# Kernel optimization log

Hardware: AMD Instinct MI355X
Metric: run time of the kernel (lower is better)

## Reference

```python
import jax, jax.numpy as jnp
import numpy as np

B, S, H, NH, HD = 1, 2048, 768, 12, 64   # batch, seq, hidden, heads, head_dim
W = 256                                   # one-sided window (attention_window=512)
NC = S // W                               # query chunks of width W
L, FF, V, G = 12, 3072, 50265, 1          # layers, ffn, vocab, num global tokens (CLS)
HID, EMB = 768, 256                       # head dense size, output embedding size
SCALE = 1.0 / np.sqrt(HD).astype(np.float32)
EPS = 1e-5

def _ln(x, s, b):
    mu = x.mean(-1, keepdims=True)
    xm = x - mu
    v = (xm * xm).mean(-1, keepdims=True)
    return xm * jax.lax.rsqrt(v + EPS) * s + b

def _forward(input_ids, attention_mask, global_attention_mask,
             word_emb, pos_emb, emb_ln_s, emb_ln_b,
             Wq, bq, Wk, bk, Wv, bv, Wqg, bqg, Wkg, bkg, Wvg, bvg, Wo, bo,
             ln1_s, ln1_b, Wf1, bf1, Wf2, bf2, ln2_s, ln2_b,
             dense_w, dense_b, out_w, out_b):
    h = word_emb[input_ids] + pos_emb[None]            # [B,S,H]
    h = _ln(h, emb_ln_s, emb_ln_b)

    key_ok = attention_mask.astype(bool)               # [B,S]
    is_glb = global_attention_mask.astype(bool)        # [B,S]

    # chunked sliding-window machinery: queries in NC chunks of W, each sees 3W keys
    j = jnp.arange(3 * W); qi = jnp.arange(W); c = jnp.arange(NC)
    rel = j[None, :] - qi[:, None]
    band_ok = (rel >= 0) & (rel <= 2 * W)              # |key-query| <= W  -> [W,3W]
    kpos = c[:, None, None] * W + j[None, None, :] - W # abs key position [NC,1,3W]
    in_range = (kpos >= 0) & (kpos < S)
    kposc = jnp.clip(kpos, 0, S - 1)
    # HF removes global tokens from the windowed band (they get dedicated columns)
    kmask = key_ok[:, kposc] & ~is_glb[:, kposc]       # [B,NC,1,3W]
    band_mask = band_ok[None, None] & in_range[None] & kmask          # [B,NC,W,3W]
    gcol_mask = jnp.broadcast_to(key_ok[:, None, None, :G], (B, NC, W, G))
    full_mask = jnp.concatenate([gcol_mask, band_mask], -1)[:, None]  # [B,1,NC,W,G+3W]
    kidx = c[:, None] * W + j[None, :]                 # gather into padded keys [NC,3W]

    def step(h, p):
        q = ((h @ p['Wq'] + p['bq']).reshape(B, NC, W, NH, HD)) * SCALE
        k = (h @ p['Wk'] + p['bk']).reshape(B, S, NH, HD)
        v = (h @ p['Wv'] + p['bv']).reshape(B, S, NH, HD)
        k_ch = jnp.pad(k, ((0, 0), (W, W), (0, 0), (0, 0)))[:, kidx]  # [B,NC,3W,NH,HD]
        v_ch = jnp.pad(v, ((0, 0), (W, W), (0, 0), (0, 0)))[:, kidx]
        s_band = jnp.einsum('bcqnd,bcknd->bncqk', q, k_ch)            # [B,NH,NC,W,3W]
        s_glob = jnp.einsum('bcqnd,bgnd->bncqg', q, k[:, :G])         # [B,NH,NC,W,G]
        scores = jnp.concatenate([s_glob, s_band], -1)
        probs = jax.nn.softmax(jnp.where(full_mask, scores, -1e9), -1)
        pg, pb = probs[..., :G], probs[..., G:]
        out = (jnp.einsum('bncqk,bcknd->bcqnd', pb, v_ch)
               + jnp.einsum('bncqg,bgnd->bcqnd', pg, v[:, :G]))
        out = out.reshape(B, S, NH, HD)
        # global tokens: full attention with dedicated global projections (HF semantics)
        hg = h[:, :G]
        qg = ((hg @ p['Wqg'] + p['bqg']).reshape(B, G, NH, HD)) * SCALE
        kg = (h @ p['Wkg'] + p['bkg']).reshape(B, S, NH, HD)
        vg = (h @ p['Wvg'] + p['bvg']).reshape(B, S, NH, HD)
        sg = jnp.einsum('bgnd,bsnd->bngs', qg, kg)
        ag = jax.nn.softmax(jnp.where(key_ok[:, None, None, :], sg, -1e9), -1)
        og = jnp.einsum('bngs,bsnd->bgnd', ag, vg)
        out = out.at[:, :G].set(og)
        attn = out.reshape(B, S, H) @ p['Wo'] + p['bo']
        h2 = _ln(h + attn, p['ln1_s'], p['ln1_b'])
        ff = jax.nn.gelu(h2 @ p['Wf1'] + p['bf1'], approximate=False) @ p['Wf2'] + p['bf2']
        return _ln(h2 + ff, p['ln2_s'], p['ln2_b']), None

    params = dict(Wq=Wq, bq=bq, Wk=Wk, bk=bk, Wv=Wv, bv=bv, Wqg=Wqg, bqg=bqg,
                  Wkg=Wkg, bkg=bkg, Wvg=Wvg, bvg=bvg, Wo=Wo, bo=bo,
                  ln1_s=ln1_s, ln1_b=ln1_b, Wf1=Wf1, bf1=bf1, Wf2=Wf2, bf2=bf2,
                  ln2_s=ln2_s, ln2_b=ln2_b)
    h, _ = jax.lax.scan(step, h, params)
    pooled = h[:, 0]                                   # CLS token
    y = jnp.tanh(pooled @ dense_w + dense_b)           # dropout = identity (eval)
    return y @ out_w + out_b                           # [B,EMB]

def setup_inputs() -> dict:
    key = jax.random.key(0)
    it = iter(jax.random.split(key, 16))
    def nrm(shape, sd=0.02):
        return jax.random.normal(next(it), shape, jnp.float32) * sd
    return dict(
        input_ids=jax.random.randint(next(it), (B, S), 0, V),
        attention_mask=jnp.ones((B, S), jnp.int32),
        global_attention_mask=jnp.zeros((B, S), jnp.int32).at[:, 0].set(1),
        word_emb=nrm((V, H)), pos_emb=nrm((S, H)),
        emb_ln_s=jnp.ones((H,)), emb_ln_b=jnp.zeros((H,)),
        Wq=nrm((L, H, H)), bq=jnp.zeros((L, H)),
        Wk=nrm((L, H, H)), bk=jnp.zeros((L, H)),
        Wv=nrm((L, H, H)), bv=jnp.zeros((L, H)),
        Wqg=nrm((L, H, H)), bqg=jnp.zeros((L, H)),
        Wkg=nrm((L, H, H)), bkg=jnp.zeros((L, H)),
        Wvg=nrm((L, H, H)), bvg=jnp.zeros((L, H)),
        Wo=nrm((L, H, H)), bo=jnp.zeros((L, H)),
        ln1_s=jnp.ones((L, H)), ln1_b=jnp.zeros((L, H)),
        Wf1=nrm((L, H, FF)), bf1=jnp.zeros((L, FF)),
        Wf2=nrm((L, FF, H)), bf2=jnp.zeros((L, H)),
        ln2_s=jnp.ones((L, H)), ln2_b=jnp.zeros((L, H)),
        dense_w=nrm((H, HID)), dense_b=jnp.zeros((HID,)),
        out_w=nrm((HID, EMB)), out_b=jnp.zeros((EMB,)),
    )

def reference(input_ids, attention_mask, global_attention_mask,
              word_emb, pos_emb, emb_ln_s, emb_ln_b,
              Wq, bq, Wk, bk, Wv, bv, Wqg, bqg, Wkg, bkg, Wvg, bvg, Wo, bo,
              ln1_s, ln1_b, Wf1, bf1, Wf2, bf2, ln2_s, ln2_b,
              dense_w, dense_b, out_w, out_b):
    return _forward(input_ids, attention_mask, global_attention_mask,
                    word_emb, pos_emb, emb_ln_s, emb_ln_b,
                    Wq, bq, Wk, bk, Wv, bv, Wqg, bqg, Wkg, bkg, Wvg, bvg, Wo, bo,
                    ln1_s, ln1_b, Wf1, bf1, Wf2, bf2, ln2_s, ln2_b,
                    dense_w, dense_b, out_w, out_b)
```

## Files before the change

### kernel.cpp

```cpp
#include <hip/hip_runtime.h>
#include <hip/hip_bf16.h>

typedef __hip_bfloat16 bf16;
using bf16x8 = __attribute__((ext_vector_type(8))) short;
using f32x4  = __attribute__((ext_vector_type(4))) float;

#define kNEG 1.0e9f

__device__ __forceinline__ float b2f(bf16 x){ return __bfloat162float(x); }
__device__ __forceinline__ bf16  f2b(float x){ return __float2bfloat16(x); }

#define GLDS16(gp, lp) __builtin_amdgcn_global_load_lds( \
    (const __attribute__((address_space(1))) void*)(gp), \
    (__attribute__((address_space(3))) void*)(lp), 16, 0, 0)

__device__ __forceinline__ void unpack8(uint4 u, float* f){
  f[0]=__uint_as_float(u.x<<16); f[1]=__uint_as_float(u.x&0xffff0000u);
  f[2]=__uint_as_float(u.y<<16); f[3]=__uint_as_float(u.y&0xffff0000u);
  f[4]=__uint_as_float(u.z<<16); f[5]=__uint_as_float(u.z&0xffff0000u);
  f[6]=__uint_as_float(u.w<<16); f[7]=__uint_as_float(u.w&0xffff0000u);
}

__global__ __launch_bounds__(256)
void embed_ln(const int* __restrict__ ids, const float* __restrict__ wemb,
              const float* __restrict__ pemb, const float* __restrict__ lns,
              const float* __restrict__ lnb, float* __restrict__ hout,
              bf16* __restrict__ hbout)
{
  const int row = blockIdx.x;
  const int tid = threadIdx.x;
  const int wave = tid >> 6, lane = tid & 63;
  const int id = ids[row];
  float x[3];
  #pragma unroll
  for (int p=0;p<3;p++){
    int i = tid + p*256;
    x[p] = wemb[(size_t)id*768 + i] + pemb[(size_t)row*768 + i];
  }
  float s1 = x[0]+x[1]+x[2];
  float s2 = x[0]*x[0]+x[1]*x[1]+x[2]*x[2];
  #pragma unroll
  for (int m=32;m>=1;m>>=1){ s1 += __shfl_xor(s1,m); s2 += __shfl_xor(s2,m); }
  __shared__ float red[8];
  if (lane==0){ red[wave]=s1; red[4+wave]=s2; }
  __syncthreads();
  s1 = red[0]+red[1]+red[2]+red[3];
  s2 = red[4]+red[5]+red[6]+red[7];
  float mu = s1*(1.0f/768.0f);
  float var = s2*(1.0f/768.0f) - mu*mu;
  float rs = rsqrtf(var + 1e-5f);
  #pragma unroll
  for (int p=0;p<3;p++){
    int i = tid + p*256;
    float y = (x[p]-mu)*rs*lns[i] + lnb[i];
    hout[(size_t)row*768+i] = y;
    hbout[(size_t)row*768+i] = f2b(y);
  }
}

__global__ __launch_bounds__(256)
void add_ln(const float* __restrict__ res, const float* __restrict__ d0,
            const float* __restrict__ d1,
            const float* __restrict__ lns, const float* __restrict__ lnb,
            float* __restrict__ hout, bf16* __restrict__ hbout)
{
  const int row = blockIdx.x;
  const int tid = threadIdx.x;
  const int wave = tid >> 6, lane = tid & 63;
  float x[3];
  #pragma unroll
  for (int p=0;p<3;p++){
    int i = tid + p*256;
    size_t idx = (size_t)row*768+i;
    x[p] = res[idx] + d0[idx] + d1[idx];
  }
  float s1 = x[0]+x[1]+x[2];
  float s2 = x[0]*x[0]+x[1]*x[1]+x[2]*x[2];
  #pragma unroll
  for (int m=32;m>=1;m>>=1){ s1 += __shfl_xor(s1,m); s2 += __shfl_xor(s2,m); }
  __shared__ float red[8];
  if (lane==0){ red[wave]=s1; red[4+wave]=s2; }
  __syncthreads();
  s1 = red[0]+red[1]+red[2]+red[3];
  s2 = red[4]+red[5]+red[6]+red[7];
  float mu = s1*(1.0f/768.0f);
  float var = s2*(1.0f/768.0f) - mu*mu;
  float rs = rsqrtf(var + 1e-5f);
  #pragma unroll
  for (int p=0;p<3;p++){
    int i = tid + p*256;
    float y = (x[p]-mu)*rs*lns[i] + lnb[i];
    hout[(size_t)row*768+i] = y;
    hbout[(size_t)row*768+i] = f2b(y);
  }
}

__global__ __launch_bounds__(256)
void prep_all(const float* __restrict__ Wq, const float* __restrict__ Wk,
              const float* __restrict__ Wv, const float* __restrict__ Wkg,
              const float* __restrict__ Wvg, const float* __restrict__ Wo,
              const float* __restrict__ Wf1, const float* __restrict__ Wf2,
              const float* __restrict__ bq, const float* __restrict__ bk,
              const float* __restrict__ bv, const float* __restrict__ bkg,
              const float* __restrict__ bvg,
              bf16* __restrict__ WcatT, bf16* __restrict__ WoT,
              bf16* __restrict__ Wf1T, bf16* __restrict__ Wf2T,
              float* __restrict__ bcat)
{
  const int b = blockIdx.x;
  const int l = blockIdx.y;
  const int tid = threadIdx.x;
  const size_t oHH = (size_t)l*768*768;
  const size_t oHF = (size_t)l*768*3072;
  const size_t oH  = (size_t)l*768;
  if (b >= 504) {
    int i = (b-504)*256 + tid;
    int which = i / 768, j = i - which*768;
    float v;
    if      (which==0) v = bq[oH+j] * 0.125f;
    else if (which==1) v = bk[oH+j];
    else if (which==2) v = bv[oH+j];
    else if (which==3) v = bkg[oH+j];
    else               v = bvg[oH+j];
    bcat[(size_t)l*3840 + i] = v;
    return;
  }
  const float* src; bf16* dst; int N, KT64, p0, tk, k0, n0; float scale = 1.0f;
  if (b < 180) {
    int wsel = b/36, tile = b - wsel*36;
    int tkk = tile/3, tn = tile - tkk*3;
    if      (wsel==0){ src=Wq+oHH;  scale=0.125f; }
    else if (wsel==1){ src=Wk+oHH; }
    else if (wsel==2){ src=Wv+oHH; }
    else if (wsel==3){ src=Wkg+oHH; }
    else             { src=Wvg+oHH; }
    dst = WcatT + (size_t)l*5*768*768;
    N=768; KT64=12; k0=tkk*64; n0=tn*256; p0 = wsel*6 + tn*2; tk = tkk;
  } else if (b < 216) {
    int tile = b-180, tkk = tile/3, tn = tile - tkk*3;
    src = Wo+oHH; dst = WoT + (size_t)l*768*768;
    N=768; KT64=12; k0=tkk*64; n0=tn*256; p0 = tn*2; tk = tkk;
  } else if (b < 360) {
    int tile = b-216, tkk = tile/12, tn = tile - tkk*12;
    src = Wf1+oHF; dst = Wf1T + (size_t)l*768*3072;
    N=3072; KT64=12; k0=tkk*64; n0=tn*256; p0 = tn*2; tk = tkk;
  } else {
    int tile = b-360, tkk = tile/3, tn = tile - tkk*3;
    src = Wf2+oHF; dst = Wf2T + (size_t)l*768*3072;
    N=768; KT64=48; k0=tkk*64; n0=tn*256; p0 = tn*2; tk = tkk;
  }

  __shared__ bf16 t[64][264];
  const int wave = tid>>6, lane = tid&63;
  float4 v[16];
  #pragma unroll
  for (int i=0;i<16;i++){
    int r = i*4 + wave;
    v[i] = *(const float4*)&src[(size_t)(k0+r)*N + n0 + lane*4];
  }
  #pragma unroll
  for (int i=0;i<16;i++){
    int r = i*4 + wave;
    union { ushort4 u; bf16 h[4]; } pk;
    pk.h[0]=f2b(v[i].x*scale); pk.h[1]=f2b(v[i].y*scale);
    pk.h[2]=f2b(v[i].z*scale); pk.h[3]=f2b(v[i].w*scale);
    *(ushort4*)&t[r][lane*4] = pk.u;
  }
  __syncthreads();
  const int rr = tid>>1, half = tid&1;
  const int r7 = rr & 7;
  #pragma unroll
  for (int c=0;c<4;c++){
    const int pp = c>>1, tt = c&1;
    union { uint4 u[2]; bf16 h[16]; } pk;
    #pragma unroll
    for (int j=0;j<16;j++)
      pk.h[j] = t[tt*32 + half*16 + j][pp*128 + rr];
    bf16* base = dst + ((size_t)(p0+pp)*KT64 + tk)*8192 + rr*64;
    const int g0 = tt*4 + half*2;
    *(uint4*)(base + (((g0  ) ^ r7)<<3)) = pk.u[0];
    *(uint4*)(base + (((g0+1) ^ r7)<<3)) = pk.u[1];
  }
}

template<int OUTF, int OUTB, int GELU, int KSPLIT, int VT>
__global__ __launch_bounds__(256)
void gemm_bt(const bf16* __restrict__ A, const bf16* __restrict__ Bt,
             const float* __restrict__ bias,
             float* __restrict__ outf, bf16* __restrict__ outb,
             bf16* __restrict__ vt,
             int M, int N, int K)
{
  __shared__ bf16 As[2][128*64];
  __shared__ bf16 Bs[2][128*64];
  const int tid  = threadIdx.x;
  const int lane = tid & 63;
  const int wave = tid >> 6;
  const int wm = wave >> 1, wn = wave & 1;
  const int gx = gridDim.x, nwg = gx*gridDim.y;
  const int w  = blockIdx.y*gx + blockIdx.x;
  const int cpx = nwg >> 3;
  const int sw = (w & 7)*cpx + (w >> 3);
  const int bm = sw % gx, bn = sw / gx;
  const int bz = (KSPLIT>1) ? blockIdx.z : 0;
  const int fr = lane & 15;
  const int fk = lane >> 4;
  const int x7 = fr & 7;
  const int Ks = K / KSPLIT;
  const int nt = Ks >> 6;
  const int kbeg = bz * Ks;
  const int KT64 = K >> 6;

  const bf16* pa[4];
  int ldsA[4];
  #pragma unroll
  for (int i=0;i<4;i++){
    int s = i*256 + tid;
    int row = s >> 3, k8l = s & 7;
    pa[i] = A + (size_t)(bm*128 + row)*K + kbeg + ((k8l ^ (row&7))<<3);
    ldsA[i] = s*8;
  }
  const bf16* pB = Bt + ((size_t)bn*KT64 + (kbeg>>6))*8192;

  f32x4 acc[4][4];
  const f32x4 zero = {0.f,0.f,0.f,0.f};
  #pragma unroll
  for (int i=0;i<4;i++)
    #pragma unroll
    for (int j=0;j<4;j++) acc[i][j] = zero;

  #pragma unroll
  for (int i=0;i<4;i++) GLDS16(pa[i], &As[0][ldsA[i]]);
  #pragma unroll
  for (int i=0;i<4;i++){ int o=(i*256+tid)*8; GLDS16(pB+o, &Bs[0][o]); }
  if (nt > 1) {
    #pragma unroll
    for (int i=0;i<4;i++) GLDS16(pa[i]+64, &As[1][ldsA[i]]);
    #pragma unroll
    for (int i=0;i<4;i++){ int o=(i*256+tid)*8; GLDS16(pB+8192+o, &Bs[1][o]); }
  }

  for (int t = 0; t < nt; ++t) {
    const int cur = t & 1;
    if (t < nt-1) asm volatile("s_waitcnt vmcnt(8)" ::: "memory");
    else          asm volatile("s_waitcnt vmcnt(0)" ::: "memory");
    __builtin_amdgcn_s_barrier();
    __builtin_amdgcn_sched_barrier(0);

    bf16x8 af[2][4], bfr[2][4];
    #pragma unroll
    for (int kk=0;kk<2;kk++){
      #pragma unroll
      for (int m=0;m<4;m++)
        af[kk][m] = *reinterpret_cast<const bf16x8*>(
            &As[cur][(wm*64 + m*16 + fr)*64 + ((((kk<<2)+fk) ^ x7)<<3)]);
      #pragma unroll
      for (int n=0;n<4;n++)
        bfr[kk][n] = *reinterpret_cast<const bf16x8*>(
            &Bs[cur][(wn*64 + n*16 + fr)*64 + ((((kk<<2)+fk) ^ x7)<<3)]);
    }
    #pragma unroll
    for (int kk=0;kk<2;kk++)
      #pragma unroll
      for (int m=0;m<4;m++)
        #pragma unroll
        for (int n=0;n<4;n++)
          acc[m][n] = __builtin_amdgcn_mfma_f32_16x16x32_bf16(af[kk][m], bfr[kk][n], acc[m][n], 0,0,0);

    __builtin_amdgcn_s_barrier();
    __builtin_amdgcn_sched_barrier(0);
    if (t+2 < nt) {
      #pragma unroll
      for (int i=0;i<4;i++) GLDS16(pa[i] + (size_t)(t+2)*64, &As[cur][ldsA[i]]);
      #pragma unroll
      for (int i=0;i<4;i++){ int o=(i*256+tid)*8;
        GLDS16(pB + (size_t)(t+2)*8192 + o, &Bs[cur][o]); }
    }
  }

  const int row0 = bm*128 + wm*64 + (lane>>4)*4;
  const int col0 = bn*128 + wn*64 + fr;
  float* outfz = OUTF ? (outf + (size_t)bz*M*N) : nullptr;
  #pragma unroll
  for (int n=0;n<4;n++){
    const int col = col0 + n*16;
    const float bv = (bz==0) ? bias[col] : 0.f;
    #pragma unroll
    for (int m=0;m<4;m++){
      const int r0 = row0 + m*16;
      union { ushort4 u; bf16 h[4]; } pk;
      #pragma unroll
      for (int r=0;r<4;r++){
        float x = acc[m][n][r] + bv;
        if (GELU) x = 0.5f*x*(1.0f + erff(x*0.70710678118f));
        size_t idx = (size_t)(r0+r)*N + col;
        pk.h[r] = f2b(x);
        if (OUTF) outfz[idx] = x;
        if (OUTB) outb[idx] = pk.h[r];
      }
      if (VT) {
        if (col >= 1536 && col < 2304)
          *(ushort4*)&vt[(size_t)(col-1536)*2048 + r0] = pk.u;
      }
    }
  }
}

__global__ __launch_bounds__(256)
void band_attn(const bf16* __restrict__ qkv, const bf16* __restrict__ Vt,
               const float* __restrict__ h0, const float* __restrict__ Wqg,
               const float* __restrict__ bqg,
               const int* __restrict__ amask, const int* __restrict__ gmask,
               bf16* __restrict__ attn)
{
  const int c = blockIdx.x, n = blockIdx.y, rg = blockIdx.z;
  const int tid = threadIdx.x, wave = tid>>6, lane = tid&63;

  if (rg == 4) {
    if (c != 0) return;
    __shared__ float sg[2048];
    __shared__ float qh[64];
    __shared__ float redg[8];
    __shared__ float partg[4][64];
    {
      const int d = tid & 63;
      const int w = tid >> 6;
      const float* wp = Wqg + (size_t)(w*192)*768 + n*64 + d;
      float a = 0.f;
      #pragma unroll 8
      for (int k=0;k<192;k++) a += h0[w*192+k] * wp[(size_t)k*768];
      partg[w][d] = a;
    }
    __syncthreads();
    if (tid < 64)
      qh[tid] = (partg[0][tid]+partg[1][tid]+partg[2][tid]+partg[3][tid] + bqg[n*64+tid]) * 0.125f;
    __syncthreads();

    float smax = -3.0e38f;
    for (int p=0;p<8;p++){
      int s = p*256 + tid;
      const uint4* kr = (const uint4*)(qkv + (size_t)s*3840 + 2304 + n*64);
      float acc = 0.f;
      #pragma unroll
      for (int d8=0; d8<8; d8++){
        float f[8]; unpack8(kr[d8], f);
        #pragma unroll
        for (int e=0;e<8;e++) acc += f[e]*qh[d8*8+e];
      }
      if (amask[s] == 0) acc = -kNEG;
      sg[s] = acc;
      smax = fmaxf(smax, acc);
    }
    #pragma unroll
    for (int mk=32; mk>=1; mk>>=1) smax = fmaxf(smax, __shfl_xor(smax, mk));
    if (lane==0) redg[wave] = smax;
    __syncthreads();
    smax = fmaxf(fmaxf(redg[0],redg[1]),fmaxf(redg[2],redg[3]));
    float ssum = 0.f;
    for (int p=0;p<8;p++){
      int s = p*256 + tid;
      float e = __expf(sg[s]-smax);
      sg[s] = e;
      ssum += e;
    }
    #pragma unroll
    for (int mk=32; mk>=1; mk>>=1) ssum += __shfl_xor(ssum, mk);
    if (lane==0) redg[4+wave] = ssum;
    __syncthreads();
    float total = redg[4]+redg[5]+redg[6]+redg[7];
    __syncthreads();

    float o0=0.f,o1=0.f,o2=0.f,o3=0.f;
    const int base = wave*512;
    for (int s = base; s < base+512; s+=4){
      o0 += sg[s]   * b2f(qkv[(size_t)s*3840     + 3072 + n*64 + lane]);
      o1 += sg[s+1] * b2f(qkv[(size_t)(s+1)*3840 + 3072 + n*64 + lane]);
      o2 += sg[s+2] * b2f(qkv[(size_t)(s+2)*3840 + 3072 + n*64 + lane]);
      o3 += sg[s+3] * b2f(qkv[(size_t)(s+3)*3840 + 3072 + n*64 + lane]);
    }
    partg[wave][lane] = (o0+o1)+(o2+o3);
    __syncthreads();
    if (tid < 64) {
      float oo = (partg[0][tid]+partg[1][tid]+partg[2][tid]+partg[3][tid]) / total;
      attn[n*64+tid] = f2b(oo);
    }
    return;
  }

  const int fr = lane & 15, fk = lane >> 4;
  const int jj = tid >> 2, seg = tid & 3;

  __shared__ __attribute__((aligned(16))) bf16 q_s[64][72];
  __shared__ __attribute__((aligned(16))) bf16 k_s[2][64][72];
  __shared__ __attribute__((aligned(16))) bf16 vt_s[2][64][72];
  __shared__ __attribute__((aligned(16))) bf16 p_s[4][16][72];
  __shared__ int  okk_s[768];
  __shared__ float kv0[2][64];

  {
    const uint4* src = (const uint4*)(qkv + (size_t)(c*256 + rg*64 + jj)*3840 + n*64 + seg*16);
    *(uint4*)&q_s[jj][seg*16]   = src[0];
    *(uint4*)&q_s[jj][seg*16+8] = src[1];
  }
  #pragma unroll
  for (int p=0;p<3;p++){
    int j = tid + p*256;
    int kpos = c*256 + j - 256;
    int ok = 0;
    if (kpos >= 0 && kpos < 2048) ok = (amask[kpos] != 0) && (gmask[kpos] == 0);
    okk_s[j] = ok;
  }
  if (tid < 64)       kv0[0][tid]    = b2f(qkv[768  + n*64 + tid]);
  else if (tid < 128) kv0[1][tid-64] = b2f(qkv[1536 + n*64 + (tid-64)]);

  auto loadK = [&](int kt, uint4& a, uint4& b){
    int kpos = c*256 + kt*64 + jj - 256;
    int kq = kpos < 0 ? 0 : (kpos > 2047 ? 2047 : kpos);
    const uint4* ks = (const uint4*)(qkv + (size_t)kq*3840 + 768 + n*64 + seg*16);
    a = ks[0]; b = ks[1];
  };
  auto loadV = [&](int kt, uint4& a, uint4& b){
    int base = c*256 + kt*64 - 256;
    int sb = (base < 0 || base > 2048-64) ? 0 : base;
    const uint4* vs = (const uint4*)(Vt + (size_t)(n*64 + jj)*2048 + sb + seg*8);
    a = vs[0]; b = vs[4];
  };

  uint4 ka,kb,va,vb;
  loadK(rg,ka,kb); loadV(rg,va,vb);
  *(uint4*)&k_s[0][jj][seg*16]    = ka;
  *(uint4*)&k_s[0][jj][seg*16+8]  = kb;
  *(uint4*)&vt_s[0][jj][seg*8]    = va;
  *(uint4*)&vt_s[0][jj][seg*8+32] = vb;

  float m[4], l[4];
  f32x4 out[4];
  const f32x4 zero = {0.f,0.f,0.f,0.f};
  #pragma unroll
  for (int r=0;r<4;r++){ m[r] = -kNEG; l[r] = 0.f; }
  #pragma unroll
  for (int dt=0;dt<4;dt++) out[dt] = zero;

  const int kt1 = (rg+8 < 11) ? rg+8 : 11;
  int cur = 0;
  for (int kt = rg; kt <= kt1; kt++) {
    const bool pf = (kt < kt1);
    if (pf){ loadK(kt+1,ka,kb); loadV(kt+1,va,vb); }
    __syncthreads();

    f32x4 s[4];
    #pragma unroll
    for (int ct=0;ct<4;ct++) s[ct] = zero;
    #pragma unroll
    for (int ks=0;ks<2;ks++){
      bf16x8 aq = *reinterpret_cast<const bf16x8*>(&q_s[wave*16 + fr][ks*32 + fk*8]);
      #pragma unroll
      for (int ct=0;ct<4;ct++){
        bf16x8 bk = *reinterpret_cast<const bf16x8*>(&k_s[cur][ct*16 + fr][ks*32 + fk*8]);
        s[ct] = __builtin_amdgcn_mfma_f32_16x16x32_bf16(aq, bk, s[ct], 0,0,0);
      }
    }
    const int qbase = rg*64 + wave*16 + fk*4;
    #pragma unroll
    for (int ct=0;ct<4;ct++){
      int j = kt*64 + ct*16 + fr;
      int okj = okk_s[j];
      #pragma unroll
      for (int r=0;r<4;r++){
        unsigned rel = (unsigned)(j - (qbase + r));
        s[ct][r] = (okj && rel <= 512u) ? s[ct][r] : -kNEG;
      }
    }
    float fac[4], psum[4];
    #pragma unroll
    for (int r=0;r<4;r++){
      float mm = fmaxf(fmaxf(s[0][r], s[1][r]), fmaxf(s[2][r], s[3][r]));
      #pragma unroll
      for (int mk=8; mk>=1; mk>>=1) mm = fmaxf(mm, __shfl_xor(mm, mk));
      float mn = fmaxf(m[r], mm);
      fac[r] = __expf(m[r] - mn);
      m[r] = mn;
      psum[r] = 0.f;
    }
    #pragma unroll
    for (int ct=0;ct<4;ct++){
      #pragma unroll
      for (int r=0;r<4;r++){
        float p = __expf(s[ct][r] - m[r]);
        psum[r] += p;
        p_s[wave][fk*4 + r][ct*16 + fr] = f2b(p);
      }
    }
    #pragma unroll
    for (int r=0;r<4;r++){
      float ts = psum[r];
      #pragma unroll
      for (int mk=8; mk>=1; mk>>=1) ts += __shfl_xor(ts, mk);
      l[r] = l[r]*fac[r] + ts;
    }
    #pragma unroll
    for (int dt=0;dt<4;dt++)
      #pragma unroll
      for (int r=0;r<4;r++) out[dt][r] *= fac[r];
    #pragma unroll
    for (int ks=0;ks<2;ks++){
      bf16x8 ap = *reinterpret_cast<const bf16x8*>(&p_s[wave][fr][ks*32 + fk*8]);
      #pragma unroll
      for (int dt=0;dt<4;dt++){
        bf16x8 bv = *reinterpret_cast<const bf16x8*>(&vt_s[cur][dt*16 + fr][ks*32 + fk*8]);
        out[dt] = __builtin_amdgcn_mfma_f32_16x16x32_bf16(ap, bv, out[dt], 0,0,0);
      }
    }

    if (pf){
      *(uint4*)&k_s[cur^1][jj][seg*16]    = ka;
      *(uint4*)&k_s[cur^1][jj][seg*16+8]  = kb;
      *(uint4*)&vt_s[cur^1][jj][seg*8]    = va;
      *(uint4*)&vt_s[cur^1][jj][seg*8+32] = vb;
      cur ^= 1;
    }
  }

  const bool okg = (amask[0] != 0);
  #pragma unroll
  for (int r=0;r<4;r++){
    const int row16 = fk*4 + r;
    float sp = 0.f;
    #pragma unroll
    for (int e=0;e<4;e++){
      int d = fr*4 + e;
      sp += b2f(q_s[wave*16 + row16][d]) * kv0[0][d];
    }
    #pragma unroll
    for (int mk=8; mk>=1; mk>>=1) sp += __shfl_xor(sp, mk);
    float sg2 = okg ? sp : -kNEG;
    float mn = fmaxf(m[r], sg2);
    float fc = __expf(m[r]-mn);
    float pg = __expf(sg2-mn);
    float lf = l[r]*fc + pg;
    const int srow = c*256 + rg*64 + wave*16 + row16;
    if (srow != 0) {
      #pragma unroll
      for (int dt=0;dt<4;dt++){
        int d = dt*16 + fr;
        float o = (out[dt][r]*fc + pg*kv0[1][d]) / lf;
        attn[(size_t)srow*768 + n*64 + d] = f2b(o);
      }
    }
  }
}

__global__ __launch_bounds__(768)
void head(const float* __restrict__ h0, const float* __restrict__ dw,
          const float* __restrict__ db, const float* __restrict__ ow,
          const float* __restrict__ ob, float* __restrict__ out)
{
  __shared__ float y[768];
  const int tid = threadIdx.x;
  float acc = 0.f;
  #pragma unroll 8
  for (int k=0;k<768;k++) acc += h0[k]*dw[(size_t)k*768 + tid];
  y[tid] = tanhf(acc + db[tid]);
  __syncthreads();
  if (tid < 256) {
    float a = 0.f;
    #pragma unroll 8
    for (int k=0;k<768;k++) a += y[k]*ow[(size_t)k*256 + tid];
    out[tid] = a + ob[tid];
  }
}

extern "C" void kernel_launch(void* const* d_in, const int* in_sizes, int n_in,
                              void* d_out, int out_size, void* d_ws, size_t ws_size,
                              hipStream_t stream)
{
  const int*   ids   = (const int*)d_in[0];
  const int*   amask = (const int*)d_in[1];
  const int*   gmask = (const int*)d_in[2];
  const float* wemb  = (const float*)d_in[3];
  const float* pemb  = (const float*)d_in[4];
  const float* elns  = (const float*)d_in[5];
  const float* elnb  = (const float*)d_in[6];
  const float* Wq    = (const float*)d_in[7];
  const float* bq    = (const float*)d_in[8];
  const float* Wk    = (const float*)d_in[9];
  const float* bk    = (const float*)d_in[10];
  const float* Wv    = (const float*)d_in[11];
  const float* bv    = (const float*)d_in[12];
  const float* Wqg   = (const float*)d_in[13];
  const float* bqg   = (const float*)d_in[14];
  const float* Wkg   = (const float*)d_in[15];
  const float* bkg   = (const float*)d_in[16];
  const float* Wvg   = (const float*)d_in[17];
  const float* bvg   = (const float*)d_in[18];
  const float* Wo    = (const float*)d_in[19];
  const float* bo    = (const float*)d_in[20];
  const float* ln1s  = (const float*)d_in[21];
  const float* ln1b  = (const float*)d_in[22];
  const float* Wf1   = (const float*)d_in[23];
  const float* bf1   = (const float*)d_in[24];
  const float* Wf2   = (const float*)d_in[25];
  const float* bf2   = (const float*)d_in[26];
  const float* ln2s  = (const float*)d_in[27];
  const float* ln2b  = (const float*)d_in[28];
  const float* dw    = (const float*)d_in[29];
  const float* db    = (const float*)d_in[30];
  const float* ow    = (const float*)d_in[31];
  const float* ob    = (const float*)d_in[32];

  char* ws = (char*)d_ws;
  size_t off = 0;
  auto alloc = [&](size_t bytes)->char*{
    char* p = ws + off; off += (bytes + 255) & ~(size_t)255; return p;
  };
  float* h     = (float*)alloc((size_t)2048*768*4);
  bf16*  hb    = (bf16*) alloc((size_t)2048*768*2);
  float* h2    = (float*)alloc((size_t)2048*768*4);
  bf16*  h2b   = (bf16*) alloc((size_t)2048*768*2);
  bf16*  qkv   = (bf16*) alloc((size_t)2048*3840*2);
  bf16*  att   = (bf16*) alloc((size_t)2048*768*2);
  bf16*  f1    = (bf16*) alloc((size_t)2048*3072*2);
  bf16*  Vtb   = (bf16*) alloc((size_t)768*2048*2);
  bf16*  WcatT = (bf16*) alloc((size_t)12*5*768*768*2);
  bf16*  WoT   = (bf16*) alloc((size_t)12*768*768*2);
  bf16*  Wf1T  = (bf16*) alloc((size_t)12*768*3072*2);
  bf16*  Wf2T  = (bf16*) alloc((size_t)12*768*3072*2);
  float* bcat  = (float*)alloc((size_t)12*3840*4);
  float* pf    = (float*)qkv;
  const size_t MN = (size_t)2048*768;

  prep_all<<<dim3(519,12),256,0,stream>>>(Wq, Wk, Wv, Wkg, Wvg, Wo, Wf1, Wf2,
                                          bq, bk, bv, bkg, bvg,
                                          WcatT, WoT, Wf1T, Wf2T, bcat);
  embed_ln<<<2048,256,0,stream>>>(ids, wemb, pemb, elns, elnb, h, hb);

  for (int l=0; l<12; l++) {
    const size_t oHH = (size_t)l*768*768;
    const size_t oH  = (size_t)l*768;
    const size_t oF  = (size_t)l*3072;
    const bf16* WcatT_l = WcatT + (size_t)l*5*768*768;
    const bf16* WoT_l   = WoT   + (size_t)l*768*768;
    const bf16* Wf1T_l  = Wf1T  + (size_t)l*768*3072;
    const bf16* Wf2T_l  = Wf2T  + (size_t)l*768*3072;
    const float* bcat_l = bcat  + (size_t)l*3840;

    gemm_bt<0,1,0,1,1><<<dim3(16,30),256,0,stream>>>(hb, WcatT_l, bcat_l, nullptr, qkv,
                                                     Vtb, 2048, 3840, 768);
    band_attn<<<dim3(8,12,5),256,0,stream>>>(qkv, Vtb, h, Wqg+oHH, bqg+oH,
                                             amask, gmask, att);
    gemm_bt<1,0,0,2,0><<<dim3(16,6,2),256,0,stream>>>(att, WoT_l, bo+oH, pf, nullptr,
                                                      nullptr, 2048, 768, 768);
    add_ln<<<2048,256,0,stream>>>(h, pf, pf+MN, ln1s+oH, ln1b+oH, h2, h2b);
    gemm_bt<0,1,1,1,0><<<dim3(16,24),256,0,stream>>>(h2b, Wf1T_l, bf1+oF, nullptr, f1,
                                                     nullptr, 2048, 3072, 768);
    gemm_bt<1,0,0,2,0><<<dim3(16,6,2),256,0,stream>>>(f1, Wf2T_l, bf2+oH, pf, nullptr,
                                                      nullptr, 2048, 768, 3072);
    add_ln<<<2048,256,0,stream>>>(h2, pf, pf+MN, ln2s+oH, ln2b+oH, h, hb);
  }

  head<<<1,768,0,stream>>>(h, dw, db, ow, ob, (float*)d_out);
}
```

Baseline: 2.374 ms.

## Process two weight tiles per prep block and raise MFMA wave priority

The weight-prep kernel now has each block convert two 64x256 tiles instead of one, halving the grid. The second tile's global loads are issued before the first tile's LDS transpose and store, so they overlap. Separately, s_setprio(1) now wraps the MFMA sections in the GEMM and the band-attention kernels, so matrix-issuing waves get scheduler priority over waves doing loads or softmax. The trade-off is more registers per prep thread and fewer prep blocks in flight.

```diff
diff --git a/kernel.cpp b/kernel.cpp
--- a/kernel.cpp
+++ b/kernel.cpp
@@ -113,8 +113,8 @@
   const size_t oHH = (size_t)l*768*768;
   const size_t oHF = (size_t)l*768*3072;
   const size_t oH  = (size_t)l*768;
-  if (b >= 504) {
-    int i = (b-504)*256 + tid;
+  if (b >= 252) {
+    int i = (b-252)*256 + tid;
     int which = i / 768, j = i - which*768;
     float v;
     if      (which==0) v = bq[oH+j] * 0.125f;
@@ -125,50 +125,64 @@
     bcat[(size_t)l*3840 + i] = v;
     return;
   }
-  const float* src; bf16* dst; int N, KT64, p0, tk, k0, n0; float scale = 1.0f;
-  if (b < 180) {
-    int wsel = b/36, tile = b - wsel*36;
-    int tkk = tile/3, tn = tile - tkk*3;
-    if      (wsel==0){ src=Wq+oHH;  scale=0.125f; }
-    else if (wsel==1){ src=Wk+oHH; }
-    else if (wsel==2){ src=Wv+oHH; }
-    else if (wsel==3){ src=Wkg+oHH; }
-    else             { src=Wvg+oHH; }
-    dst = WcatT + (size_t)l*5*768*768;
-    N=768; KT64=12; k0=tkk*64; n0=tn*256; p0 = wsel*6 + tn*2; tk = tkk;
-  } else if (b < 216) {
-    int tile = b-180, tkk = tile/3, tn = tile - tkk*3;
-    src = Wo+oHH; dst = WoT + (size_t)l*768*768;
-    N=768; KT64=12; k0=tkk*64; n0=tn*256; p0 = tn*2; tk = tkk;
-  } else if (b < 360) {
-    int tile = b-216, tkk = tile/12, tn = tile - tkk*12;
-    src = Wf1+oHF; dst = Wf1T + (size_t)l*768*3072;
-    N=3072; KT64=12; k0=tkk*64; n0=tn*256; p0 = tn*2; tk = tkk;
-  } else {
-    int tile = b-360, tkk = tile/3, tn = tile - tkk*3;
-    src = Wf2+oHF; dst = Wf2T + (size_t)l*768*3072;
-    N=768; KT64=48; k0=tkk*64; n0=tn*256; p0 = tn*2; tk = tkk;
-  }
+
+  struct TP { const float* src; bf16* dst; int N, KT64, p0, tk, k0, n0; float scale; };
+  auto decode = [&](int tb)->TP{
+    TP P; P.scale = 1.0f;
+    if (tb < 180) {
+      int wsel = tb/36, tile = tb - wsel*36;
+      int tkk = tile/3, tn = tile - tkk*3;
+      if      (wsel==0){ P.src=Wq+oHH;  P.scale=0.125f; }
+      else if (wsel==1){ P.src=Wk+oHH; }
+      else if (wsel==2){ P.src=Wv+oHH; }
+      else if (wsel==3){ P.src=Wkg+oHH; }
+      else             { P.src=Wvg+oHH; }
+      P.dst = WcatT + (size_t)l*5*768*768;
+      P.N=768; P.KT64=12; P.k0=tkk*64; P.n0=tn*256; P.p0 = wsel*6 + tn*2; P.tk = tkk;
+    } else if (tb < 216) {
+      int tile = tb-180, tkk = tile/3, tn = tile - tkk*3;
+      P.src = Wo+oHH; P.dst = WoT + (size_t)l*768*768;
+      P.N=768; P.KT64=12; P.k0=tkk*64; P.n0=tn*256; P.p0 = tn*2; P.tk = tkk;
+    } else if (tb < 360) {
+      int tile = tb-216, tkk = tile/12, tn = tile - tkk*12;
+      P.src = Wf1+oHF; P.dst = Wf1T + (size_t)l*768*3072;
+      P.N=3072; P.KT64=12; P.k0=tkk*64; P.n0=tn*256; P.p0 = tn*2; P.tk = tkk;
+    } else {
+      int tile = tb-360, tkk = tile/3, tn = tile - tkk*3;
+      P.src = Wf2+oHF; P.dst = Wf2T + (size_t)l*768*3072;
+      P.N=768; P.KT64=48; P.k0=tkk*64; P.n0=tn*256; P.p0 = tn*2; P.tk = tkk;
+    }
+    return P;
+  };
+  const TP A = decode(2*b);
+  const TP B = decode(2*b+1);
 
   __shared__ bf16 t[64][264];
   const int wave = tid>>6, lane = tid&63;
+  const int rr = tid>>1, half = tid&1;
+  const int r7 = rr & 7;
+
   float4 v[16];
   #pragma unroll
   for (int i=0;i<16;i++){
     int r = i*4 + wave;
-    v[i] = *(const float4*)&src[(size_t)(k0+r)*N + n0 + lane*4];
+    v[i] = *(const float4*)&A.src[(size_t)(A.k0+r)*A.N + A.n0 + lane*4];
   }
   #pragma unroll
   for (int i=0;i<16;i++){
     int r = i*4 + wave;
     union { ushort4 u; bf16 h[4]; } pk;
-    pk.h[0]=f2b(v[i].x*scale); pk.h[1]=f2b(v[i].y*scale);
-    pk.h[2]=f2b(v[i].z*scale); pk.h[3]=f2b(v[i].w*scale);
+    pk.h[0]=f2b(v[i].x*A.scale); pk.h[1]=f2b(v[i].y*A.scale);
+    pk.h[2]=f2b(v[i].z*A.scale); pk.h[3]=f2b(v[i].w*A.scale);
     *(ushort4*)&t[r][lane*4] = pk.u;
   }
   __syncthreads();
-  const int rr = tid>>1, half = tid&1;
-  const int r7 = rr & 7;
+  float4 w[16];
+  #pragma unroll
+  for (int i=0;i<16;i++){
+    int r = i*4 + wave;
+    w[i] = *(const float4*)&B.src[(size_t)(B.k0+r)*B.N + B.n0 + lane*4];
+  }
   #pragma unroll
   for (int c=0;c<4;c++){
     const int pp = c>>1, tt = c&1;
@@ -176,7 +190,29 @@
     #pragma unroll
     for (int j=0;j<16;j++)
       pk.h[j] = t[tt*32 + half*16 + j][pp*128 + rr];
-    bf16* base = dst + ((size_t)(p0+pp)*KT64 + tk)*8192 + rr*64;
+    bf16* base = A.dst + ((size_t)(A.p0+pp)*A.KT64 + A.tk)*8192 + rr*64;
+    const int g0 = tt*4 + half*2;
+    *(uint4*)(base + (((g0  ) ^ r7)<<3)) = pk.u[0];
+    *(uint4*)(base + (((g0+1) ^ r7)<<3)) = pk.u[1];
+  }
+  __syncthreads();
+  #pragma unroll
+  for (int i=0;i<16;i++){
+    int r = i*4 + wave;
+    union { ushort4 u; bf16 h[4]; } pk;
+    pk.h[0]=f2b(w[i].x*B.scale); pk.h[1]=f2b(w[i].y*B.scale);
+    pk.h[2]=f2b(w[i].z*B.scale); pk.h[3]=f2b(w[i].w*B.scale);
+    *(ushort4*)&t[r][lane*4] = pk.u;
+  }
+  __syncthreads();
+  #pragma unroll
+  for (int c=0;c<4;c++){
+    const int pp = c>>1, tt = c&1;
+    union { uint4 u[2]; bf16 h[16]; } pk;
+    #pragma unroll
+    for (int j=0;j<16;j++)
+      pk.h[j] = t[tt*32 + half*16 + j][pp*128 + rr];
+    bf16* base = B.dst + ((size_t)(B.p0+pp)*B.KT64 + B.tk)*8192 + rr*64;
     const int g0 = tt*4 + half*2;
     *(uint4*)(base + (((g0  ) ^ r7)<<3)) = pk.u[0];
     *(uint4*)(base + (((g0+1) ^ r7)<<3)) = pk.u[1];
@@ -259,6 +295,7 @@
         bfr[kk][n] = *reinterpret_cast<const bf16x8*>(
             &Bs[cur][(wn*64 + n*16 + fr)*64 + ((((kk<<2)+fk) ^ x7)<<3)]);
     }
+    __builtin_amdgcn_s_setprio(1);
     #pragma unroll
     for (int kk=0;kk<2;kk++)
       #pragma unroll
@@ -266,6 +303,7 @@
         #pragma unroll
         for (int n=0;n<4;n++)
           acc[m][n] = __builtin_amdgcn_mfma_f32_16x16x32_bf16(af[kk][m], bfr[kk][n], acc[m][n], 0,0,0);
+    __builtin_amdgcn_s_setprio(0);
 
     __builtin_amdgcn_s_barrier();
     __builtin_amdgcn_sched_barrier(0);
@@ -451,6 +489,7 @@
     f32x4 s[4];
     #pragma unroll
     for (int ct=0;ct<4;ct++) s[ct] = zero;
+    __builtin_amdgcn_s_setprio(1);
     #pragma unroll
     for (int ks=0;ks<2;ks++){
       bf16x8 aq = *reinterpret_cast<const bf16x8*>(&q_s[wave*16 + fr][ks*32 + fk*8]);
@@ -460,6 +499,7 @@
         s[ct] = __builtin_amdgcn_mfma_f32_16x16x32_bf16(aq, bk, s[ct], 0,0,0);
       }
     }
+    __builtin_amdgcn_s_setprio(0);
     const int qbase = rg*64 + wave*16 + fk*4;
     #pragma unroll
     for (int ct=0;ct<4;ct++){
@@ -502,6 +542,7 @@
     for (int dt=0;dt<4;dt++)
       #pragma unroll
       for (int r=0;r<4;r++) out[dt][r] *= fac[r];
+    __builtin_amdgcn_s_setprio(1);
     #pragma unroll
     for (int ks=0;ks<2;ks++){
       bf16x8 ap = *reinterpret_cast<const bf16x8*>(&p_s[wave][fr][ks*32 + fk*8]);
@@ -511,6 +552,7 @@
         out[dt] = __builtin_amdgcn_mfma_f32_16x16x32_bf16(ap, bv, out[dt], 0,0,0);
       }
     }
+    __builtin_amdgcn_s_setprio(0);
 
     if (pf){
       *(uint4*)&k_s[cur^1][jj][seg*16]    = ka;
@@ -629,7 +671,7 @@
   float* pf    = (float*)qkv;
   const size_t MN = (size_t)2048*768;
 
-  prep_all<<<dim3(519,12),256,0,stream>>>(Wq, Wk, Wv, Wkg, Wvg, Wo, Wf1, Wf2,
+  prep_all<<<dim3(267,12),256,0,stream>>>(Wq, Wk, Wv, Wkg, Wvg, Wo, Wf1, Wf2,
                                           bq, bk, bv, bkg, bvg,
                                           WcatT, WoT, Wf1T, Wf2T, bcat);
   embed_ln<<<2048,256,0,stream>>>(ids, wemb, pemb, elns, elnb, h, hb);
```

Measured after the change: 2.386 ms. No clear change (+0.5%).
